# Performance work log

Hardware: AMD Instinct MI355X
Metric: run time of the kernel (lower is better)

Reference implementation:

```python
import jax, jax.numpy as jnp
import numpy as np

N_EMBD = 384
N_HEAD = 6
HEAD_SIZE = N_EMBD // N_HEAD  # 64
BLOCK = 64
EPS = 1e-5


def _layernorm(x, g, b):
    mu = jnp.mean(x, axis=-1, keepdims=True)
    var = jnp.mean(jnp.square(x - mu), axis=-1, keepdims=True)
    return (x - mu) * jax.lax.rsqrt(var + EPS) * g + b


def setup_inputs() -> dict:
    key = jax.random.key(0)
    ks = jax.random.split(key, 12)
    s = 0.02
    return {
        "x": jax.random.normal(ks[0], (1024, BLOCK, N_EMBD), dtype=jnp.float32),
        "ln1_g": jnp.ones((N_EMBD,), jnp.float32),
        "ln1_b": jnp.zeros((N_EMBD,), jnp.float32),
        "Wq": jax.random.normal(ks[1], (N_HEAD, N_EMBD, HEAD_SIZE), jnp.float32) * s,
        "Wk": jax.random.normal(ks[2], (N_HEAD, N_EMBD, HEAD_SIZE), jnp.float32) * s,
        "Wv": jax.random.normal(ks[3], (N_HEAD, N_EMBD, HEAD_SIZE), jnp.float32) * s,
        "Wo": jax.random.normal(ks[4], (N_EMBD, N_EMBD), jnp.float32) * s,
        "bo": jnp.zeros((N_EMBD,), jnp.float32),
        "ln2_g": jnp.ones((N_EMBD,), jnp.float32),
        "ln2_b": jnp.zeros((N_EMBD,), jnp.float32),
        "W1": jax.random.normal(ks[5], (N_EMBD, 4 * N_EMBD), jnp.float32) * s,
        "b1": jnp.zeros((4 * N_EMBD,), jnp.float32),
        "W2": jax.random.normal(ks[6], (4 * N_EMBD, N_EMBD), jnp.float32) * s,
        "b2": jnp.zeros((N_EMBD,), jnp.float32),
    }


def reference(x, ln1_g, ln1_b, Wq, Wk, Wv, Wo, bo, ln2_g, ln2_b, W1, b1, W2, b2):
    B, T, C = x.shape
    # --- multi-head causal self-attention on ln1(x) ---
    xn = _layernorm(x, ln1_g, ln1_b)
    q = jnp.einsum('btc,hcd->bhtd', xn, Wq)
    k = jnp.einsum('btc,hcd->bhtd', xn, Wk)
    v = jnp.einsum('btc,hcd->bhtd', xn, Wv)
    scale = HEAD_SIZE ** -0.5
    att = jnp.einsum('bhtd,bhsd->bhts', q, k) * scale
    causal = jnp.tril(jnp.ones((T, T), bool))
    att = jnp.where(causal, att, -jnp.inf)
    att = jax.nn.softmax(att, axis=-1)  # dropout is identity at eval
    out = jnp.einsum('bhts,bhsd->bhtd', att, v)
    out = out.transpose(0, 2, 1, 3).reshape(B, T, C)  # concat heads
    x = x + out @ Wo + bo
    # --- feed-forward on ln2(x) ---
    xn2 = _layernorm(x, ln2_g, ln2_b)
    h = jax.nn.relu(xn2 @ W1 + b1)
    x = x + h @ W2 + b2
    return x
```

## Files before the change

### kernel.cpp

```cpp
#include <hip/hip_runtime.h>

#define TT 64
#define CC 384
#define NH 6
#define HID 1536
#define LDX 392
#define LDH 72
#define LDS_H 264

typedef __bf16 bf16x8 __attribute__((ext_vector_type(8)));
typedef float f32x4 __attribute__((ext_vector_type(4)));
typedef unsigned short us8 __attribute__((ext_vector_type(8)));

#define MFMA(a, b, c) __builtin_amdgcn_mfma_f32_16x16x32_bf16(a, b, c, 0, 0, 0)
#define WAITVM(N) asm volatile("s_waitcnt vmcnt(" #N ")" ::: "memory")

static __device__ __forceinline__ unsigned short f2bf(float f) {
  unsigned u = __builtin_bit_cast(unsigned, f);
  u += 0x7FFFu + ((u >> 16) & 1u);
  return (unsigned short)(u >> 16);
}
static __device__ __forceinline__ float bf2f(unsigned short h) {
  unsigned u = ((unsigned)h) << 16;
  return __builtin_bit_cast(float, u);
}
static __device__ __forceinline__ bf16x8 ld8(const unsigned short* p) {
  return __builtin_bit_cast(bf16x8, *reinterpret_cast<const us8*>(p));
}
static __device__ __forceinline__ void glds16(const unsigned short* g, unsigned short* l) {
  __builtin_amdgcn_global_load_lds(
      (const __attribute__((address_space(1))) void*)g,
      (__attribute__((address_space(3))) void*)l, 16, 0, 0);
}

__global__ void prep_w(const float* __restrict__ Wq, const float* __restrict__ Wk,
                       const float* __restrict__ Wv, const float* __restrict__ Wo,
                       const float* __restrict__ W1, const float* __restrict__ W2,
                       unsigned short* __restrict__ ws) {
  const int T0 = 1152 * 384;
  const int T1 = T0 + 384 * 384;
  const int T2 = T1 + 1536 * 384;
  const int T3 = T2 + 384 * 1536;
  for (int i = blockIdx.x * blockDim.x + threadIdx.x; i < T3; i += gridDim.x * blockDim.x) {
    float v;
    if (i < T0) {
      int n = i / 384, k = i % 384;
      int hh = n / 192, j = n % 192;
      const float* W = (j < 64) ? Wq : (j < 128) ? Wk : Wv;
      int d = (j < 64) ? j : (j < 128) ? j - 64 : j - 128;
      v = W[((size_t)hh * 384 + k) * 64 + d];
    } else if (i < T1) {
      int i2 = i - T0; int n = i2 / 384, k = i2 % 384;
      v = Wo[(size_t)k * 384 + n];
    } else if (i < T2) {
      int i2 = i - T1; int n = i2 / 384, k = i2 % 384;
      v = W1[(size_t)k * 1536 + n];
    } else {
      int i2 = i - T2; int n = i2 / 1536, k = i2 % 1536;
      v = W2[(size_t)k * 384 + n];
    }
    ws[i] = f2bf(v);
  }
}

__global__ __launch_bounds__(256, 2)
void attn_fwd(const float* __restrict__ x,
              const float* __restrict__ ln1g, const float* __restrict__ ln1b,
              const float* __restrict__ bo,
              const unsigned short* __restrict__ Wqkv,
              const unsigned short* __restrict__ WoT,
              float* __restrict__ x2) {
  __shared__ unsigned short sXN[TT * LDX];
  __shared__ unsigned short sHEAD[3 * TT * LDH];
  unsigned short* sQ = sHEAD;
  unsigned short* sK = sHEAD + TT * LDH;
  unsigned short* sV = sHEAD + 2 * TT * LDH;

  const int b = blockIdx.x;
  const int tid = threadIdx.x;
  const int wv = tid >> 6;
  const int ln = tid & 63;
  const int l16 = ln & 15;
  const int lg = ln >> 4;
  const float* xb = x + (size_t)b * TT * CC;
  const f32x4 Z4 = {0.f, 0.f, 0.f, 0.f};

#pragma unroll 1
  for (int r = wv * 16; r < wv * 16 + 16; ++r) {
    float v[6], s = 0.f, sq = 0.f;
#pragma unroll
    for (int j = 0; j < 6; ++j) { v[j] = xb[r * CC + ln + 64 * j]; s += v[j]; sq += v[j] * v[j]; }
#pragma unroll
    for (int off = 32; off; off >>= 1) { s += __shfl_xor(s, off); sq += __shfl_xor(sq, off); }
    float mu = s * (1.f / CC);
    float rs = rsqrtf(sq * (1.f / CC) - mu * mu + 1e-5f);
#pragma unroll
    for (int j = 0; j < 6; ++j) {
      int c = ln + 64 * j;
      sXN[r * LDX + c] = f2bf((v[j] - mu) * rs * ln1g[c] + ln1b[c]);
    }
  }
  __syncthreads();

  f32x4 pacc[4][6];
#pragma unroll
  for (int m = 0; m < 4; ++m)
#pragma unroll
    for (int c = 0; c < 6; ++c) pacc[m][c] = Z4;

  const unsigned short* prow[6];
#pragma unroll
  for (int c = 0; c < 6; ++c)
    prow[c] = WoT + (size_t)(wv * 96 + c * 16 + l16) * CC + 8 * lg;

#pragma unroll 1
  for (int h = 0; h < NH; ++h) {
    const unsigned short* wrow[3];
#pragma unroll
    for (int c = 0; c < 3; ++c)
      wrow[c] = Wqkv + (size_t)(h * 192 + wv * 48 + c * 16 + l16) * CC + 8 * lg;

    f32x4 qacc[4][3];
#pragma unroll
    for (int m = 0; m < 4; ++m)
#pragma unroll
      for (int c = 0; c < 3; ++c) qacc[m][c] = Z4;

    bf16x8 bpre[2][3];
#pragma unroll
    for (int c = 0; c < 3; ++c) bpre[0][c] = ld8(wrow[c] + 0);
#pragma unroll
    for (int c = 0; c < 3; ++c) bpre[1][c] = ld8(wrow[c] + 32);
#pragma unroll
    for (int kk = 0; kk < CC; kk += 32) {
      const int slot = (kk >> 5) & 1;
      bf16x8 bcur[3];
#pragma unroll
      for (int c = 0; c < 3; ++c) bcur[c] = bpre[slot][c];
      if (kk + 64 < CC) {
#pragma unroll
        for (int c = 0; c < 3; ++c) bpre[slot][c] = ld8(wrow[c] + kk + 64);
      }
      bf16x8 a[4];
#pragma unroll
      for (int m = 0; m < 4; ++m)
        a[m] = ld8(&sXN[(m * 16 + l16) * LDX + kk + 8 * lg]);
#pragma unroll
      for (int c = 0; c < 3; ++c)
#pragma unroll
        for (int m = 0; m < 4; ++m) qacc[m][c] = MFMA(a[m], bcur[c], qacc[m][c]);
    }
    __syncthreads();
#pragma unroll
    for (int m = 0; m < 4; ++m)
#pragma unroll
      for (int c = 0; c < 3; ++c) {
        int n = wv * 48 + c * 16 + l16;
#pragma unroll
        for (int rg = 0; rg < 4; ++rg) {
          int t = m * 16 + lg * 4 + rg;
          unsigned short bv = f2bf(qacc[m][c][rg]);
          if (n < 64) sQ[t * LDH + n] = bv;
          else if (n < 128) sK[t * LDH + (n - 64)] = bv;
          else sV[(n - 128) * LDH + t] = bv;
        }
      }
    __syncthreads();

    f32x4 sacc[4];
#pragma unroll
    for (int c = 0; c < 4; ++c) sacc[c] = Z4;
#pragma unroll
    for (int kk = 0; kk < 64; kk += 32) {
      bf16x8 a = ld8(&sQ[(wv * 16 + l16) * LDH + kk + 8 * lg]);
#pragma unroll
      for (int c = 0; c < 4; ++c) {
        bf16x8 bb = ld8(&sK[(c * 16 + l16) * LDH + kk + 8 * lg]);
        sacc[c] = MFMA(a, bb, sacc[c]);
      }
    }
#pragma unroll
    for (int rg = 0; rg < 4; ++rg) {
      int row = wv * 16 + lg * 4 + rg;
      float e[4], mx = -1e30f;
#pragma unroll
      for (int c = 0; c < 4; ++c) {
        int col = c * 16 + l16;
        float vv = sacc[c][rg] * 0.125f;
        e[c] = (col <= row) ? vv : -1e30f;
        mx = fmaxf(mx, e[c]);
      }
#pragma unroll
      for (int off = 8; off; off >>= 1) mx = fmaxf(mx, __shfl_xor(mx, off));
      float sum = 0.f;
#pragma unroll
      for (int c = 0; c < 4; ++c) {
        int col = c * 16 + l16;
        e[c] = (col <= row) ? __expf(e[c] - mx) : 0.f;
        sum += e[c];
      }
#pragma unroll
      for (int off = 8; off; off >>= 1) sum += __shfl_xor(sum, off);
      float inv = 1.f / sum;
#pragma unroll
      for (int c = 0; c < 4; ++c)
        sQ[row * LDH + c * 16 + l16] = f2bf(e[c] * inv);
    }

    bf16x8 pb[2][6];
#pragma unroll
    for (int s2 = 0; s2 < 2; ++s2)
#pragma unroll
      for (int c = 0; c < 6; ++c)
        pb[s2][c] = ld8(prow[c] + h * 64 + 32 * s2);

    f32x4 oacc[4];
#pragma unroll
    for (int c = 0; c < 4; ++c) oacc[c] = Z4;
#pragma unroll
    for (int kk = 0; kk < 64; kk += 32) {
      bf16x8 a = ld8(&sQ[(wv * 16 + l16) * LDH + kk + 8 * lg]);
#pragma unroll
      for (int c = 0; c < 4; ++c) {
        bf16x8 bb = ld8(&sV[(c * 16 + l16) * LDH + kk + 8 * lg]);
        oacc[c] = MFMA(a, bb, oacc[c]);
      }
    }
    __syncthreads();
#pragma unroll
    for (int c = 0; c < 4; ++c)
#pragma unroll
      for (int rg = 0; rg < 4; ++rg) {
        int t = wv * 16 + lg * 4 + rg;
        sK[t * LDH + c * 16 + l16] = f2bf(oacc[c][rg]);
      }
    __syncthreads();

#pragma unroll
    for (int kk = 0; kk < 64; kk += 32) {
      const int slot = kk >> 5;
      bf16x8 a[4];
#pragma unroll
      for (int m = 0; m < 4; ++m)
        a[m] = ld8(&sK[(m * 16 + l16) * LDH + kk + 8 * lg]);
#pragma unroll
      for (int c = 0; c < 6; ++c)
#pragma unroll
        for (int m = 0; m < 4; ++m) pacc[m][c] = MFMA(a[m], pb[slot][c], pacc[m][c]);
    }
  }

  float* xo = x2 + (size_t)b * TT * CC;
#pragma unroll
  for (int m = 0; m < 4; ++m)
#pragma unroll
    for (int c = 0; c < 6; ++c) {
      int n = wv * 96 + c * 16 + l16;
      float bov = bo[n];
#pragma unroll
      for (int rg = 0; rg < 4; ++rg) {
        int t = m * 16 + lg * 4 + rg;
        xo[t * CC + n] = xb[t * CC + n] + pacc[m][c][rg] + bov;
      }
    }
}

__global__ __launch_bounds__(512, 2)
void mlp_fwd(const float* __restrict__ ln2g, const float* __restrict__ ln2b,
             const float* __restrict__ b1, const float* __restrict__ b2,
             const unsigned short* __restrict__ W1T,
             const unsigned short* __restrict__ W2T,
             float* xo) {
  __shared__ unsigned short sXN[TT * LDX];
  __shared__ unsigned short sH[TT * LDS_H];
  __shared__ unsigned short sW[8 * 4096];

  const int b = blockIdx.x;
  const int tid = threadIdx.x;
  const int wv = tid >> 6;
  const int ln = tid & 63;
  const int l16 = ln & 15;
  const int lg = ln >> 4;
  float* xb = xo + (size_t)b * TT * CC;
  const f32x4 Z4 = {0.f, 0.f, 0.f, 0.f};
  unsigned short* myW = sW + (wv << 12);

#pragma unroll 1
  for (int r = wv * 8; r < wv * 8 + 8; ++r) {
    float v[6], s = 0.f, sq = 0.f;
#pragma unroll
    for (int j = 0; j < 6; ++j) { v[j] = xb[r * CC + ln + 64 * j]; s += v[j]; sq += v[j] * v[j]; }
#pragma unroll
    for (int off = 32; off; off >>= 1) { s += __shfl_xor(s, off); sq += __shfl_xor(sq, off); }
    float mu = s * (1.f / CC);
    float rs = rsqrtf(sq * (1.f / CC) - mu * mu + 1e-5f);
#pragma unroll
    for (int j = 0; j < 6; ++j) {
      int c = ln + 64 * j;
      sXN[r * LDX + c] = f2bf((v[j] - mu) * rs * ln2g[c] + ln2b[c]);
    }
  }
  __syncthreads();

  const int w1_row = (wv << 5) + (ln >> 3);
  const int w1_kp0 = (((ln & 7) ^ (ln >> 3)) << 3);
  const int w2_row = wv * 48 + (ln >> 2);
  const int w2_kp0 = ((((ln & 3) ^ ((ln >> 3) & 3))) << 3);

  f32x4 macc[4][3];
#pragma unroll
  for (int m = 0; m < 4; ++m)
#pragma unroll
    for (int c = 0; c < 3; ++c) macc[m][c] = Z4;

#pragma unroll 1
  for (int ch = 0; ch < 6; ++ch) {
    f32x4 hacc[4][2];
#pragma unroll
    for (int m = 0; m < 4; ++m)
#pragma unroll
      for (int c = 0; c < 2; ++c) hacc[m][c] = Z4;

    {
      const unsigned short* g = W1T + (size_t)(ch * 256 + w1_row) * CC + 0 * 64 + w1_kp0;
      unsigned short* d = myW + 0 * 2048;
#pragma unroll
      for (int j = 0; j < 4; ++j) glds16(g + (size_t)(j * 8) * CC, d + (j << 9));
    }
    int cb = 0;
#pragma unroll 1
    for (int s = 0; s < 6; ++s) {
      if (s < 5) {
        const unsigned short* g = W1T + (size_t)(ch * 256 + w1_row) * CC + (s + 1) * 64 + w1_kp0;
        unsigned short* d = myW + (cb ^ 1) * 2048;
#pragma unroll
        for (int j = 0; j < 4; ++j) glds16(g + (size_t)(j * 8) * CC, d + (j << 9));
        WAITVM(4);
      } else {
        WAITVM(0);
      }
#pragma unroll
      for (int kk2 = 0; kk2 < 2; ++kk2) {
        bf16x8 a[4];
#pragma unroll
        for (int m = 0; m < 4; ++m)
          a[m] = ld8(&sXN[(m * 16 + l16) * LDX + s * 64 + kk2 * 32 + 8 * lg]);
#pragma unroll
        for (int c = 0; c < 2; ++c) {
          int rloc = (c << 4) + l16;
          bf16x8 bb = ld8(&myW[cb * 2048 + rloc * 64 + ((kk2 * 32 + 8 * lg) ^ ((l16 & 7) << 3))]);
#pragma unroll
          for (int m = 0; m < 4; ++m) hacc[m][c] = MFMA(a[m], bb, hacc[m][c]);
        }
      }
      cb ^= 1;
    }
    __syncthreads();

    {
      const unsigned short* g = W2T + (size_t)w2_row * HID + ch * 256 + 0 * 32 + w2_kp0;
      unsigned short* d = myW + 0 * 1536;
#pragma unroll
      for (int j = 0; j < 3; ++j) glds16(g + (size_t)(j * 16) * HID, d + (j << 9));
    }
#pragma unroll
    for (int m = 0; m < 4; ++m)
#pragma unroll
      for (int c = 0; c < 2; ++c) {
        int nl = (wv << 5) + (c << 4) + l16;
        float b1v = b1[ch * 256 + nl];
#pragma unroll
        for (int rg = 0; rg < 4; ++rg) {
          int t = m * 16 + lg * 4 + rg;
          sH[t * LDS_H + nl] = f2bf(fmaxf(hacc[m][c][rg] + b1v, 0.f));
        }
      }
    __syncthreads();

    cb = 0;
#pragma unroll 1
    for (int s = 0; s < 8; ++s) {
      if (s < 7) {
        const unsigned short* g = W2T + (size_t)w2_row * HID + ch * 256 + (s + 1) * 32 + w2_kp0;
        unsigned short* d = myW + (cb ^ 1) * 1536;
#pragma unroll
        for (int j = 0; j < 3; ++j) glds16(g + (size_t)(j * 16) * HID, d + (j << 9));
        WAITVM(3);
      } else {
        WAITVM(0);
      }
      bf16x8 a[4];
#pragma unroll
      for (int m = 0; m < 4; ++m)
        a[m] = ld8(&sH[(m * 16 + l16) * LDS_H + s * 32 + 8 * lg]);
#pragma unroll
      for (int c = 0; c < 3; ++c) {
        int rloc = (c << 4) + l16;
        bf16x8 bb = ld8(&myW[cb * 1536 + rloc * 32 + ((8 * lg) ^ (((rloc >> 1) & 3) << 3))]);
#pragma unroll
        for (int m = 0; m < 4; ++m) macc[m][c] = MFMA(a[m], bb, macc[m][c]);
      }
      cb ^= 1;
    }
  }

#pragma unroll
  for (int m = 0; m < 4; ++m)
#pragma unroll
    for (int c = 0; c < 3; ++c) {
      int n = wv * 48 + c * 16 + l16;
      float b2v = b2[n];
#pragma unroll
      for (int rg = 0; rg < 4; ++rg) {
        int t = m * 16 + lg * 4 + rg;
        size_t idx = (size_t)t * CC + n;
        float x2v = xb[idx];
        xb[idx] = x2v + macc[m][c][rg] + b2v;
      }
    }
}

extern "C" void kernel_launch(void* const* d_in, const int* in_sizes, int n_in,
                              void* d_out, int out_size, void* d_ws, size_t ws_size,
                              hipStream_t stream) {
  const float* x    = (const float*)d_in[0];
  const float* ln1g = (const float*)d_in[1];
  const float* ln1b = (const float*)d_in[2];
  const float* Wq   = (const float*)d_in[3];
  const float* Wk   = (const float*)d_in[4];
  const float* Wv   = (const float*)d_in[5];
  const float* Wo   = (const float*)d_in[6];
  const float* bo   = (const float*)d_in[7];
  const float* ln2g = (const float*)d_in[8];
  const float* ln2b = (const float*)d_in[9];
  const float* W1   = (const float*)d_in[10];
  const float* b1   = (const float*)d_in[11];
  const float* W2   = (const float*)d_in[12];
  const float* b2   = (const float*)d_in[13];
  unsigned short* ws = (unsigned short*)d_ws;

  const size_t need = (size_t)(1152 * 384 + 384 * 384 + 1536 * 384 + 384 * 1536) * 2;
  if (ws_size < need) return;

  hipLaunchKernelGGL(prep_w, dim3(1024), dim3(256), 0, stream, Wq, Wk, Wv, Wo, W1, W2, ws);

  const unsigned short* Wqkv = ws;
  const unsigned short* WoT  = ws + 1152 * 384;
  const unsigned short* W1T  = WoT + 384 * 384;
  const unsigned short* W2T  = W1T + 1536 * 384;
  int nblk = in_sizes[0] / (TT * CC);

  hipLaunchKernelGGL(attn_fwd, dim3(nblk), dim3(256), 0, stream,
                     x, ln1g, ln1b, bo, Wqkv, WoT, (float*)d_out);
  hipLaunchKernelGGL(mlp_fwd, dim3(nblk), dim3(512), 0, stream,
                     ln2g, ln2b, b1, b2, W1T, W2T, (float*)d_out);
}
```

Before: 468.4 us.

## Process two sequences per MLP block with finer hidden chunks and setprio

The MLP kernel now handles 128 rows (two batch elements) per workgroup, which halves the grid. The hidden dimension is processed in 64-wide chunks over 24 iterations, and the 8 waves split into 2 row groups by 4 column slices for the W1 stage. Each W2 weight fragment is reused across 8 M-tiles instead of 4, which halves W2 global traffic per row. Shared-memory padding is replaced with XOR swizzles. s_setprio is raised around MFMA bursts in both kernels. In exchange, register pressure rises from the 8x3 accumulators, there are more barriers per chunk, and the grid is smaller.

Result: no change. 471.1 us (+0.6%).

```diff
diff --git a/kernel.cpp b/kernel.cpp
--- a/kernel.cpp
+++ b/kernel.cpp
@@ -6,7 +6,6 @@
 #define HID 1536
 #define LDX 392
 #define LDH 72
-#define LDS_H 264
 
 typedef __bf16 bf16x8 __attribute__((ext_vector_type(8)));
 typedef float f32x4 __attribute__((ext_vector_type(4)));
@@ -145,10 +144,12 @@
 #pragma unroll
       for (int m = 0; m < 4; ++m)
         a[m] = ld8(&sXN[(m * 16 + l16) * LDX + kk + 8 * lg]);
+      __builtin_amdgcn_s_setprio(1);
 #pragma unroll
       for (int c = 0; c < 3; ++c)
 #pragma unroll
         for (int m = 0; m < 4; ++m) qacc[m][c] = MFMA(a[m], bcur[c], qacc[m][c]);
+      __builtin_amdgcn_s_setprio(0);
     }
     __syncthreads();
 #pragma unroll
@@ -236,6 +237,7 @@
       }
     __syncthreads();
 
+    __builtin_amdgcn_s_setprio(1);
 #pragma unroll
     for (int kk = 0; kk < 64; kk += 32) {
       const int slot = kk >> 5;
@@ -248,6 +250,7 @@
 #pragma unroll
         for (int m = 0; m < 4; ++m) pacc[m][c] = MFMA(a[m], pb[slot][c], pacc[m][c]);
     }
+    __builtin_amdgcn_s_setprio(0);
   }
 
   float* xo = x2 + (size_t)b * TT * CC;
@@ -271,22 +274,24 @@
              const unsigned short* __restrict__ W1T,
              const unsigned short* __restrict__ W2T,
              float* xo) {
-  __shared__ unsigned short sXN[TT * LDX];
-  __shared__ unsigned short sH[TT * LDS_H];
-  __shared__ unsigned short sW[8 * 4096];
-
-  const int b = blockIdx.x;
+  __shared__ unsigned short sXN[128 * 384];
+  __shared__ unsigned short sH[128 * 64];
+  __shared__ unsigned short sW[8 * 3072];
+
+  const int bp = blockIdx.x;
   const int tid = threadIdx.x;
   const int wv = tid >> 6;
   const int ln = tid & 63;
   const int l16 = ln & 15;
   const int lg = ln >> 4;
-  float* xb = xo + (size_t)b * TT * CC;
+  const int g = wv >> 2;
+  const int p = wv & 3;
+  float* xb = xo + (size_t)bp * 128 * CC;
   const f32x4 Z4 = {0.f, 0.f, 0.f, 0.f};
-  unsigned short* myW = sW + (wv << 12);
-
-#pragma unroll 1
-  for (int r = wv * 8; r < wv * 8 + 8; ++r) {
+  unsigned short* myW = sW + wv * 3072;
+
+#pragma unroll 1
+  for (int r = wv * 16; r < wv * 16 + 16; ++r) {
     float v[6], s = 0.f, sq = 0.f;
 #pragma unroll
     for (int j = 0; j < 6; ++j) { v[j] = xb[r * CC + ln + 64 * j]; s += v[j]; sq += v[j] * v[j]; }
@@ -297,45 +302,41 @@
 #pragma unroll
     for (int j = 0; j < 6; ++j) {
       int c = ln + 64 * j;
-      sXN[r * LDX + c] = f2bf((v[j] - mu) * rs * ln2g[c] + ln2b[c]);
+      sXN[r * 384 + (c ^ ((r & 7) << 3))] = f2bf((v[j] - mu) * rs * ln2g[c] + ln2b[c]);
     }
   }
   __syncthreads();
 
-  const int w1_row = (wv << 5) + (ln >> 3);
-  const int w1_kp0 = (((ln & 7) ^ (ln >> 3)) << 3);
-  const int w2_row = wv * 48 + (ln >> 2);
-  const int w2_kp0 = ((((ln & 3) ^ ((ln >> 3) & 3))) << 3);
-
-  f32x4 macc[4][3];
-#pragma unroll
-  for (int m = 0; m < 4; ++m)
+  const int w1r = ln >> 3;
+  const int w1k = ((ln & 7) ^ (ln >> 3)) << 3;
+  const int w2r = ln >> 2;
+  const int w2k = (((ln & 3) ^ ((ln >> 3) & 3))) << 3;
+  const int rsw = (l16 & 7) << 3;
+
+  f32x4 macc[8][3];
+#pragma unroll
+  for (int m = 0; m < 8; ++m)
 #pragma unroll
     for (int c = 0; c < 3; ++c) macc[m][c] = Z4;
 
 #pragma unroll 1
-  for (int ch = 0; ch < 6; ++ch) {
-    f32x4 hacc[4][2];
-#pragma unroll
-    for (int m = 0; m < 4; ++m)
-#pragma unroll
-      for (int c = 0; c < 2; ++c) hacc[m][c] = Z4;
-
-    {
-      const unsigned short* g = W1T + (size_t)(ch * 256 + w1_row) * CC + 0 * 64 + w1_kp0;
-      unsigned short* d = myW + 0 * 2048;
-#pragma unroll
-      for (int j = 0; j < 4; ++j) glds16(g + (size_t)(j * 8) * CC, d + (j << 9));
-    }
+  for (int ch = 0; ch < 24; ++ch) {
+    f32x4 hacc[4];
+#pragma unroll
+    for (int m = 0; m < 4; ++m) hacc[m] = Z4;
+
+    const unsigned short* w1g = W1T + (size_t)(ch * 64 + p * 16 + w1r) * CC + w1k;
+#pragma unroll
+    for (int j = 0; j < 2; ++j) glds16(w1g + (size_t)(j * 8) * CC, myW + j * 512);
     int cb = 0;
 #pragma unroll 1
     for (int s = 0; s < 6; ++s) {
       if (s < 5) {
-        const unsigned short* g = W1T + (size_t)(ch * 256 + w1_row) * CC + (s + 1) * 64 + w1_kp0;
-        unsigned short* d = myW + (cb ^ 1) * 2048;
-#pragma unroll
-        for (int j = 0; j < 4; ++j) glds16(g + (size_t)(j * 8) * CC, d + (j << 9));
-        WAITVM(4);
+        const unsigned short* gsrc = w1g + (s + 1) * 64;
+        unsigned short* d = myW + (cb ^ 1) * 1024;
+#pragma unroll
+        for (int j = 0; j < 2; ++j) glds16(gsrc + (size_t)(j * 8) * CC, d + j * 512);
+        WAITVM(2);
       } else {
         WAITVM(0);
       }
@@ -344,68 +345,62 @@
         bf16x8 a[4];
 #pragma unroll
         for (int m = 0; m < 4; ++m)
-          a[m] = ld8(&sXN[(m * 16 + l16) * LDX + s * 64 + kk2 * 32 + 8 * lg]);
-#pragma unroll
-        for (int c = 0; c < 2; ++c) {
-          int rloc = (c << 4) + l16;
-          bf16x8 bb = ld8(&myW[cb * 2048 + rloc * 64 + ((kk2 * 32 + 8 * lg) ^ ((l16 & 7) << 3))]);
-#pragma unroll
-          for (int m = 0; m < 4; ++m) hacc[m][c] = MFMA(a[m], bb, hacc[m][c]);
+          a[m] = ld8(&sXN[(g * 64 + m * 16 + l16) * 384 + ((s * 64 + kk2 * 32 + 8 * lg) ^ rsw)]);
+        bf16x8 bb = ld8(&myW[cb * 1024 + l16 * 64 + ((kk2 * 32 + 8 * lg) ^ rsw)]);
+        __builtin_amdgcn_s_setprio(1);
+#pragma unroll
+        for (int m = 0; m < 4; ++m) hacc[m] = MFMA(a[m], bb, hacc[m]);
+        __builtin_amdgcn_s_setprio(0);
+      }
+      cb ^= 1;
+    }
+    __syncthreads();
+
+    const unsigned short* w2g = W2T + (size_t)(wv * 48 + w2r) * HID + ch * 64 + w2k;
+#pragma unroll
+    for (int j = 0; j < 3; ++j) glds16(w2g + (size_t)(j * 16) * HID, myW + j * 512);
+
+    {
+      float b1v = b1[ch * 64 + p * 16 + l16];
+#pragma unroll
+      for (int m = 0; m < 4; ++m)
+#pragma unroll
+        for (int rg = 0; rg < 4; ++rg) {
+          int row = g * 64 + m * 16 + lg * 4 + rg;
+          int col = p * 16 + l16;
+          sH[row * 64 + (col ^ ((row & 7) << 3))] = f2bf(fmaxf(hacc[m][rg] + b1v, 0.f));
         }
-      }
-      cb ^= 1;
-    }
-    __syncthreads();
-
-    {
-      const unsigned short* g = W2T + (size_t)w2_row * HID + ch * 256 + 0 * 32 + w2_kp0;
-      unsigned short* d = myW + 0 * 1536;
-#pragma unroll
-      for (int j = 0; j < 3; ++j) glds16(g + (size_t)(j * 16) * HID, d + (j << 9));
-    }
-#pragma unroll
-    for (int m = 0; m < 4; ++m)
-#pragma unroll
-      for (int c = 0; c < 2; ++c) {
-        int nl = (wv << 5) + (c << 4) + l16;
-        float b1v = b1[ch * 256 + nl];
-#pragma unroll
-        for (int rg = 0; rg < 4; ++rg) {
-          int t = m * 16 + lg * 4 + rg;
-          sH[t * LDS_H + nl] = f2bf(fmaxf(hacc[m][c][rg] + b1v, 0.f));
-        }
-      }
+    }
     __syncthreads();
 
     cb = 0;
 #pragma unroll 1
-    for (int s = 0; s < 8; ++s) {
-      if (s < 7) {
-        const unsigned short* g = W2T + (size_t)w2_row * HID + ch * 256 + (s + 1) * 32 + w2_kp0;
-        unsigned short* d = myW + (cb ^ 1) * 1536;
-#pragma unroll
-        for (int j = 0; j < 3; ++j) glds16(g + (size_t)(j * 16) * HID, d + (j << 9));
-        WAITVM(3);
+    for (int s = 0; s < 2; ++s) {
+      if (s == 0) {
+#pragma unroll
+        for (int j = 0; j < 3; ++j) glds16(w2g + 32 + (size_t)(j * 16) * HID, myW + 1536 + j * 512);
       } else {
         WAITVM(0);
       }
-      bf16x8 a[4];
-#pragma unroll
-      for (int m = 0; m < 4; ++m)
-        a[m] = ld8(&sH[(m * 16 + l16) * LDS_H + s * 32 + 8 * lg]);
+      bf16x8 a[8];
+#pragma unroll
+      for (int m = 0; m < 8; ++m)
+        a[m] = ld8(&sH[(m * 16 + l16) * 64 + ((s * 32 + 8 * lg) ^ rsw)]);
+      __builtin_amdgcn_s_setprio(1);
 #pragma unroll
       for (int c = 0; c < 3; ++c) {
-        int rloc = (c << 4) + l16;
+        int rloc = c * 16 + l16;
         bf16x8 bb = ld8(&myW[cb * 1536 + rloc * 32 + ((8 * lg) ^ (((rloc >> 1) & 3) << 3))]);
 #pragma unroll
-        for (int m = 0; m < 4; ++m) macc[m][c] = MFMA(a[m], bb, macc[m][c]);
-      }
+        for (int m = 0; m < 8; ++m) macc[m][c] = MFMA(a[m], bb, macc[m][c]);
+      }
+      __builtin_amdgcn_s_setprio(0);
       cb ^= 1;
     }
   }
 
 #pragma unroll
-  for (int m = 0; m < 4; ++m)
+  for (int m = 0; m < 8; ++m)
 #pragma unroll
     for (int c = 0; c < 3; ++c) {
       int n = wv * 48 + c * 16 + l16;
@@ -452,6 +447,6 @@
 
   hipLaunchKernelGGL(attn_fwd, dim3(nblk), dim3(256), 0, stream,
                      x, ln1g, ln1b, bo, Wqkv, WoT, (float*)d_out);
-  hipLaunchKernelGGL(mlp_fwd, dim3(nblk), dim3(512), 0, stream,
+  hipLaunchKernelGGL(mlp_fwd, dim3(nblk / 2), dim3(512), 0, stream,
                      ln2g, ln2b, b1, b2, W1T, W2T, (float*)d_out);
 }
```
